# Performance work log

Hardware: AMD Instinct MI355X
Metric: run time of the kernel (lower is better)

The kernel has to match this reference:

```python
import jax, jax.numpy as jnp
import numpy as np

N, C, M, P, FL = 2, 512, 8, 1, 4
SPATIAL = [(100, 100), (50, 50), (25, 25), (13, 13)]
S = sum(h * w for h, w in SPATIAL)
CM = C // M


def grid_sample_zeros(im, grid):
    """torch.nn.functional.grid_sample, bilinear, padding_mode='zeros', align_corners=False.
    im: (B, Cc, H, W); grid: (B, Hg, Wg, 2) with grid[...,0]=x, grid[...,1]=y in [-1,1].
    Returns (B, Cc, Hg, Wg)."""
    B, Cc, H, W = im.shape
    Hg, Wg = grid.shape[1], grid.shape[2]
    x = (grid[..., 0] + 1.0) * (W * 0.5) - 0.5
    y = (grid[..., 1] + 1.0) * (H * 0.5) - 0.5
    x0f = jnp.floor(x)
    y0f = jnp.floor(y)
    wx1 = x - x0f
    wy1 = y - y0f
    wx0 = 1.0 - wx1
    wy0 = 1.0 - wy1
    x0 = x0f.astype(jnp.int32)
    y0 = y0f.astype(jnp.int32)
    flat = im.reshape(B, Cc, H * W)

    def gather(ix, iy):
        valid = ((ix >= 0) & (ix < W) & (iy >= 0) & (iy < H)).astype(im.dtype)
        idx = jnp.clip(iy, 0, H - 1) * W + jnp.clip(ix, 0, W - 1)  # (B,Hg,Wg)
        idx = jnp.broadcast_to(idx.reshape(B, 1, Hg * Wg), (B, Cc, Hg * Wg))
        v = jnp.take_along_axis(flat, idx, axis=2).reshape(B, Cc, Hg, Wg)
        return v * valid[:, None]

    out = (gather(x0, y0) * (wx0 * wy0)[:, None]
           + gather(x0 + 1, y0) * (wx1 * wy0)[:, None]
           + gather(x0, y0 + 1) * (wx0 * wy1)[:, None]
           + gather(x0 + 1, y0 + 1) * (wx1 * wy1)[:, None])
    return out


def setup_inputs() -> dict:
    key = jax.random.key(0)
    ks = jax.random.split(key, 8)
    x = jax.random.normal(ks[0], (N, C, S), jnp.float32)
    pos = jax.random.normal(ks[1], (N, C, S), jnp.float32)
    key_padding_mask = jnp.zeros((N, S), jnp.bool_)
    # valid (W,H) per level; no padding -> full size, scale 1
    valid_sizes = jnp.broadcast_to(
        jnp.array([[w, h] for (h, w) in SPATIAL], jnp.float32)[None], (N, FL, 2))
    valid_scales = jnp.ones((N, FL, 2), jnp.float32)
    s = 1.0 / np.sqrt(C)
    Wv = (jax.random.normal(ks[2], (C, C), jnp.float32) * s)
    bv = jnp.zeros((C,), jnp.float32)
    Wloc = jax.random.normal(ks[3], (M * FL * P * 2, C), jnp.float32) * 0.01
    # torch bias init: head-direction grid, channel layout (M, F, P, 2)
    grid_init = np.array([-1, -1, -1, 0, -1, 1, 0, -1, 0, 1, 1, -1, 1, 0, 1, 1],
                         np.float32).reshape(M, 1, 1, 2)
    grid_init = np.tile(grid_init, (1, FL, P, 1))
    for i in range(P):
        grid_init[:, :, i, :] *= (i + 1)
    bloc = jnp.asarray(grid_init.reshape(-1))
    Ww = jax.random.normal(ks[4], (M * FL * P, C), jnp.float32) * 0.01
    bw = jnp.zeros((M * FL * P,), jnp.float32)
    Wo = (jax.random.normal(ks[5], (C, C), jnp.float32) * s)
    bo = jnp.zeros((C,), jnp.float32)
    scale = jnp.ones((C,), jnp.float32)
    return dict(x=x, pos=pos, key_padding_mask=key_padding_mask,
                valid_sizes=valid_sizes, valid_scales=valid_scales,
                Wv=Wv, bv=bv, Wloc=Wloc, bloc=bloc, Ww=Ww, bw=bw,
                Wo=Wo, bo=bo, scale=scale)


def reference(x, pos, key_padding_mask, valid_sizes, valid_scales,
              Wv, bv, Wloc, bloc, Ww, bw, Wo, bo, scale):
    mask = key_padding_mask[:, None, :]  # (N,1,S)
    x_pos = jnp.where(mask, 0.0, x + pos)
    value = jnp.einsum('oc,ncs->nos', Wv, x) + bv[:, None]
    value = jnp.where(mask, 0.0, value)

    # per-level value maps, split heads: (N*M, C/M, H, W)
    values, cur = [], 0
    for (H, W) in SPATIAL:
        values.append(value[..., cur:cur + H * W].reshape(N * M, CM, H, W))
        cur += H * W

    vs = jnp.repeat(valid_sizes, M, axis=0)          # (NM, F, 2) = repeat_interleave
    vc2 = jnp.repeat(2.0 * valid_scales, M, axis=0)  # (NM, F, 2)

    outs, cur = [], 0
    for lvl, (H, W) in enumerate(SPATIAL):
        L = H * W
        xp = x_pos[..., cur:cur + L]  # (N, C, L)
        cur += L
        # 1x1 convs == per-token linears
        off = jnp.einsum('oc,ncl->nol', Wloc, xp) + bloc[:, None]
        off = off.reshape(N * M, FL, P, 2, L).transpose(0, 1, 2, 4, 3)  # (NM,F,P,L,2)
        w = jnp.einsum('oc,ncl->nol', Ww, xp) + bw[:, None]
        w = jax.nn.softmax(w.reshape(N * M, 1, FL * P, L), axis=2)
        # pixel-center grid of the query level, (L,2) as (x,y)
        ys, xs = jnp.meshgrid(jnp.arange(H, dtype=jnp.float32) + 0.5,
                              jnp.arange(W, dtype=jnp.float32) + 0.5, indexing='ij')
        pre = jnp.stack([xs, ys], -1).reshape(L, 2)
        sc = (vc2 / vs[:, lvl:lvl + 1])[:, :, None, None, :]  # (NM,F,1,1,2)
        grids = off * sc + (pre[None, None, None] * sc - 1.0)  # (NM,F,P,L,2)
        samples = jnp.concatenate(
            [grid_sample_zeros(values[f], grids[:, f]) for f in range(FL)], axis=2)  # (NM,CM,F*P,L)
        out = jnp.sum(samples * w, axis=2).reshape(N, C, L)
        out = jnp.einsum('oc,ncl->nol', Wo, out) + bo[:, None]
        outs.append(out)
    return jnp.concatenate(outs, axis=-1) * scale[None, :, None]
```

## Files before the change

### kernel.cpp

```cpp
#include <hip/hip_runtime.h>
#include <math.h>

#define TOT_S   13294
#define NBATCH  2
#define CCH     512
#define MHEAD   8
#define PITCH   40

typedef short     short8  __attribute__((ext_vector_type(8)));
typedef float     f32x4   __attribute__((ext_vector_type(4)));
typedef unsigned short u16x8 __attribute__((ext_vector_type(8)));
typedef unsigned short u16x4 __attribute__((ext_vector_type(4)));

__device__ __forceinline__ unsigned short f2bf(float f) {
    union { float f; unsigned int u; } v; v.f = f;
    unsigned int r = v.u + 0x7fffu + ((v.u >> 16) & 1u);
    return (unsigned short)(r >> 16);
}
__device__ __forceinline__ float bf2f(unsigned short h) {
    union { unsigned int u; float f; } v; v.u = ((unsigned int)h) << 16;
    return v.f;
}

__global__ void cast_f32_bf16(const float* __restrict__ src,
                              unsigned short* __restrict__ dst, int n4)
{
    const int i = blockIdx.x * blockDim.x + threadIdx.x;
    if (i < n4) {
        const float4 v = *(const float4*)(src + (size_t)i * 4);
        u16x4 o;
        o[0] = f2bf(v.x); o[1] = f2bf(v.y); o[2] = f2bf(v.z); o[3] = f2bf(v.w);
        *(u16x4*)(dst + (size_t)i * 4) = o;
    }
}

__global__ __launch_bounds__(512)
void gemm_val_offw_mfma(const unsigned short* __restrict__ Wb,
                        const unsigned short* __restrict__ Wlb,
                        const unsigned short* __restrict__ Wwb,
                        const float* __restrict__ bv,
                        const float* __restrict__ bloc,
                        const float* __restrict__ bw,
                        const float* __restrict__ x,
                        const float* __restrict__ pos,
                        const unsigned char* __restrict__ mask,
                        unsigned short* __restrict__ valb,
                        float* __restrict__ offw)
{
    __shared__ unsigned short Wl[2][128 * PITCH];
    __shared__ unsigned short Al[2][128 * PITCH];
    const int n  = blockIdx.z;
    const int oby = blockIdx.y;
    const int sb = blockIdx.x * 128;
    const int tid = threadIdx.x;

    const int r    = tid >> 2;
    const int wh   = (tid & 3) >> 1;
    const int segh = (tid & 1) * 16;
    const int sp   = tid & 15;
    const int cgrp = (tid >> 4) & 15;
    const int half = tid >> 8;
    const size_t XLIM = (size_t)NBATCH * CCH * TOT_S - 2;

    const int wave = tid >> 6, lane = tid & 63;
    const int m0 = (wave & 1) * 64, n0 = (wave >> 1) * 32;
    const int row16 = lane & 15, q = lane >> 4;

    if (oby < 4) {
        const int ob = oby * 128;
        const unsigned short* wsrc = Wb + ((size_t)(ob + r)) * CCH + wh * 32 + segh;
        unsigned short* wdst = &Wl[wh][r * PITCH + segh];

        u16x8 w0 = *(const u16x8*)(wsrc);
        u16x8 w1 = *(const u16x8*)(wsrc + 8);
        float2 ax[2][2][2];
#pragma unroll
        for (int kh = 0; kh < 2; ++kh)
#pragma unroll
            for (int cc = 0; cc < 2; ++cc)
#pragma unroll
                for (int jj = 0; jj < 2; ++jj) {
                    size_t off = ((size_t)n * CCH + kh * 32 + 2 * cgrp + cc) * TOT_S
                               + sb + 2 * sp + 32 * (2 * half + jj);
                    off = off > XLIM ? XLIM : off;
                    ax[kh][cc][jj] = *(const float2*)(x + off);
                }

        f32x4 acc[4][2] = {};
        for (int k0 = 0; k0 < CCH; k0 += 64) {
            *(u16x8*)wdst = w0; *(u16x8*)(wdst + 8) = w1;
#pragma unroll
            for (int kh = 0; kh < 2; ++kh)
#pragma unroll
                for (int jj = 0; jj < 2; ++jj)
#pragma unroll
                    for (int i = 0; i < 2; ++i) {
                        const int s = 2 * sp + 32 * (2 * half + jj) + i;
                        const float lo = i ? ax[kh][0][jj].y : ax[kh][0][jj].x;
                        const float hi = i ? ax[kh][1][jj].y : ax[kh][1][jj].x;
                        *(unsigned int*)&Al[kh][(size_t)s * PITCH + 2 * cgrp] =
                            (unsigned int)f2bf(lo) | ((unsigned int)f2bf(hi) << 16);
                    }
            __syncthreads();
            if (k0 + 64 < CCH) {
                w0 = *(const u16x8*)(wsrc + k0 + 64);
                w1 = *(const u16x8*)(wsrc + k0 + 72);
#pragma unroll
                for (int kh = 0; kh < 2; ++kh)
#pragma unroll
                    for (int cc = 0; cc < 2; ++cc)
#pragma unroll
                        for (int jj = 0; jj < 2; ++jj) {
                            size_t off = ((size_t)n * CCH + k0 + 64 + kh * 32
                                          + 2 * cgrp + cc) * TOT_S
                                       + sb + 2 * sp + 32 * (2 * half + jj);
                            off = off > XLIM ? XLIM : off;
                            ax[kh][cc][jj] = *(const float2*)(x + off);
                        }
            }
#pragma unroll
            for (int kh = 0; kh < 2; ++kh) {
                short8 af[4], bfr[2];
#pragma unroll
                for (int mt = 0; mt < 4; ++mt)
                    af[mt] = *(const short8*)&Wl[kh][(m0 + mt * 16 + row16) * PITCH + q * 8];
#pragma unroll
                for (int nt = 0; nt < 2; ++nt)
                    bfr[nt] = *(const short8*)&Al[kh][(n0 + nt * 16 + row16) * PITCH + q * 8];
#pragma unroll
                for (int mt = 0; mt < 4; ++mt)
#pragma unroll
                    for (int nt = 0; nt < 2; ++nt)
                        acc[mt][nt] = __builtin_amdgcn_mfma_f32_16x16x32_bf16(
                            af[mt], bfr[nt], acc[mt][nt], 0, 0, 0);
            }
            __syncthreads();
        }

#pragma unroll
        for (int nt = 0; nt < 2; ++nt) {
            const int s = sb + n0 + nt * 16 + row16;
            if (s >= TOT_S) continue;
            const float msk = mask[(size_t)n * TOT_S + s] ? 0.f : 1.f;
            unsigned short* orow = valb + ((size_t)n * TOT_S + s) * CCH + ob + m0;
#pragma unroll
            for (int mt = 0; mt < 4; ++mt) {
                const f32x4 bvv = *(const f32x4*)(bv + ob + m0 + mt * 16 + q * 4);
                const f32x4 a = acc[mt][nt];
                u16x4 ov;
                ov[0] = f2bf((a[0] + bvv[0]) * msk);
                ov[1] = f2bf((a[1] + bvv[1]) * msk);
                ov[2] = f2bf((a[2] + bvv[2]) * msk);
                ov[3] = f2bf((a[3] + bvv[3]) * msk);
                *(u16x4*)(orow + mt * 16 + q * 4) = ov;
            }
        }
    } else {
        const bool wz = (r >= 96);
        const unsigned short* wsrc =
            (r < 64) ? (Wlb + (size_t)r * CCH + wh * 32 + segh)
                     : (Wwb + (size_t)((r < 96 ? r : 95) - 64) * CCH + wh * 32 + segh);
        unsigned short* wdst = &Wl[wh][r * PITCH + segh];

        float mkm[4];
#pragma unroll
        for (int jj = 0; jj < 2; ++jj)
#pragma unroll
            for (int i = 0; i < 2; ++i) {
                const int s = sb + 2 * sp + 32 * (2 * half + jj) + i;
                const int sc = s < TOT_S ? s : TOT_S - 1;
                mkm[jj * 2 + i] = mask[(size_t)n * TOT_S + sc] ? 0.f : 1.f;
            }

        u16x8 w0 = {}, w1 = {};
        if (!wz) { w0 = *(const u16x8*)(wsrc); w1 = *(const u16x8*)(wsrc + 8); }
        float2 ax[2][2][2], ap[2][2][2];
#pragma unroll
        for (int kh = 0; kh < 2; ++kh)
#pragma unroll
            for (int cc = 0; cc < 2; ++cc)
#pragma unroll
                for (int jj = 0; jj < 2; ++jj) {
                    size_t off = ((size_t)n * CCH + kh * 32 + 2 * cgrp + cc) * TOT_S
                               + sb + 2 * sp + 32 * (2 * half + jj);
                    off = off > XLIM ? XLIM : off;
                    ax[kh][cc][jj] = *(const float2*)(x + off);
                    ap[kh][cc][jj] = *(const float2*)(pos + off);
                }

        f32x4 acc[4][2] = {};
        for (int k0 = 0; k0 < CCH; k0 += 64) {
            *(u16x8*)wdst = w0; *(u16x8*)(wdst + 8) = w1;
#pragma unroll
            for (int kh = 0; kh < 2; ++kh)
#pragma unroll
                for (int jj = 0; jj < 2; ++jj)
#pragma unroll
                    for (int i = 0; i < 2; ++i) {
                        const int s = 2 * sp + 32 * (2 * half + jj) + i;
                        const float lo = (i ? ax[kh][0][jj].y + ap[kh][0][jj].y
                                            : ax[kh][0][jj].x + ap[kh][0][jj].x)
                                         * mkm[jj * 2 + i];
                        const float hi = (i ? ax[kh][1][jj].y + ap[kh][1][jj].y
                                            : ax[kh][1][jj].x + ap[kh][1][jj].x)
                                         * mkm[jj * 2 + i];
                        *(unsigned int*)&Al[kh][(size_t)s * PITCH + 2 * cgrp] =
                            (unsigned int)f2bf(lo) | ((unsigned int)f2bf(hi) << 16);
                    }
            __syncthreads();
            if (k0 + 64 < CCH) {
                if (!wz) {
                    w0 = *(const u16x8*)(wsrc + k0 + 64);
                    w1 = *(const u16x8*)(wsrc + k0 + 72);
                }
#pragma unroll
                for (int kh = 0; kh < 2; ++kh)
#pragma unroll
                    for (int cc = 0; cc < 2; ++cc)
#pragma unroll
                        for (int jj = 0; jj < 2; ++jj) {
                            size_t off = ((size_t)n * CCH + k0 + 64 + kh * 32
                                          + 2 * cgrp + cc) * TOT_S
                                       + sb + 2 * sp + 32 * (2 * half + jj);
                            off = off > XLIM ? XLIM : off;
                            ax[kh][cc][jj] = *(const float2*)(x + off);
                            ap[kh][cc][jj] = *(const float2*)(pos + off);
                        }
            }
#pragma unroll
            for (int kh = 0; kh < 2; ++kh) {
                short8 af[4], bfr[2];
#pragma unroll
                for (int mt = 0; mt < 4; ++mt)
                    af[mt] = *(const short8*)&Wl[kh][(m0 + mt * 16 + row16) * PITCH + q * 8];
#pragma unroll
                for (int nt = 0; nt < 2; ++nt)
                    bfr[nt] = *(const short8*)&Al[kh][(n0 + nt * 16 + row16) * PITCH + q * 8];
#pragma unroll
                for (int mt = 0; mt < 4; ++mt)
#pragma unroll
                    for (int nt = 0; nt < 2; ++nt)
                        acc[mt][nt] = __builtin_amdgcn_mfma_f32_16x16x32_bf16(
                            af[mt], bfr[nt], acc[mt][nt], 0, 0, 0);
            }
            __syncthreads();
        }

#pragma unroll
        for (int nt = 0; nt < 2; ++nt) {
            const int s = sb + n0 + nt * 16 + row16;
            if (s >= TOT_S) continue;
            float* orow = offw + ((size_t)n * TOT_S + s) * 96;
#pragma unroll
            for (int mt = 0; mt < 4; ++mt) {
                const int o = m0 + mt * 16 + q * 4;
                if (o < 96) {
                    const float* bsrc = (o < 64) ? (bloc + o) : (bw + o - 64);
                    const f32x4 bb = *(const f32x4*)bsrc;
                    f32x4 v = acc[mt][nt];
                    v[0] += bb[0]; v[1] += bb[1]; v[2] += bb[2]; v[3] += bb[3];
                    *(f32x4*)(orow + o) = v;
                }
            }
        }
    }
}

__global__ __launch_bounds__(256)
void sample_attn(const unsigned short* __restrict__ value,
                 const float* __restrict__ offw,
                 const float* __restrict__ vsizes,
                 const float* __restrict__ vscales,
                 unsigned short* __restrict__ samp)
{
    const int lane = threadIdx.x;
    const int item = blockIdx.x * blockDim.y + threadIdx.y;
    const int total = NBATCH * TOT_S;
    if (item >= total) return;
    const int s = item % TOT_S;
    const int n = item / TOT_S;
    const int m = lane >> 3;

    int lvl; float prex, prey;
    if (s < 10000)      { lvl = 0; const int l = s;         const int qq = l / 100; prey = qq + 0.5f; prex = (l - qq * 100) + 0.5f; }
    else if (s < 12500) { lvl = 1; const int l = s - 10000; const int qq = l / 50;  prey = qq + 0.5f; prex = (l - qq * 50)  + 0.5f; }
    else if (s < 13125) { lvl = 2; const int l = s - 12500; const int qq = l / 25;  prey = qq + 0.5f; prex = (l - qq * 25)  + 0.5f; }
    else                { lvl = 3; const int l = s - 13125; const int qq = l / 13;  prey = qq + 0.5f; prex = (l - qq * 13)  + 0.5f; }

    const float* ow = offw + ((size_t)n * TOT_S + s) * 96;

    const float w0 = ow[64 + m * 4 + 0], w1 = ow[64 + m * 4 + 1];
    const float w2 = ow[64 + m * 4 + 2], w3 = ow[64 + m * 4 + 3];
    const float mx = fmaxf(fmaxf(w0, w1), fmaxf(w2, w3));
    const float e0 = expf(w0 - mx), e1 = expf(w1 - mx), e2 = expf(w2 - mx), e3 = expf(w3 - mx);
    const float inv = 1.f / (e0 + e1 + e2 + e3);
    const float wgt[4] = { e0 * inv, e1 * inv, e2 * inv, e3 * inv };

    const int HS[4]  = { 100, 50, 25, 13 };
    const int WS[4]  = { 100, 50, 25, 13 };
    const int CUR[4] = { 0, 10000, 12500, 13125 };

    const float invsx = 1.f / vsizes[((n * 4) + lvl) * 2 + 0];
    const float invsy = 1.f / vsizes[((n * 4) + lvl) * 2 + 1];
    const unsigned short* vbase = value + (size_t)n * TOT_S * CCH + lane * 8;

    float acc[8] = {};
#pragma unroll
    for (int f = 0; f < 4; ++f) {
        const float offx = ow[(m * 4 + f) * 2 + 0];
        const float offy = ow[(m * 4 + f) * 2 + 1];
        const float scx = 2.f * vscales[((n * 4) + f) * 2 + 0] * invsx;
        const float scy = 2.f * vscales[((n * 4) + f) * 2 + 1] * invsy;
        const int Wf = WS[f], Hf = HS[f], cf = CUR[f];
        const float xi = (offx + prex) * scx * (Wf * 0.5f) - 0.5f;
        const float yi = (offy + prey) * scy * (Hf * 0.5f) - 0.5f;
        const float x0f = floorf(xi), y0f = floorf(yi);
        const float wx1 = xi - x0f, wy1 = yi - y0f;
        const float wx0 = 1.f - wx1, wy0 = 1.f - wy1;
        const int x0 = (int)x0f, y0 = (int)y0f;
        const bool xin0 = (x0 >= 0) && (x0 < Wf);
        const bool xin1 = (x0 + 1 >= 0) && (x0 + 1 < Wf);
        const bool yin0 = (y0 >= 0) && (y0 < Hf);
        const bool yin1 = (y0 + 1 >= 0) && (y0 + 1 < Hf);
        const float cw00 = (xin0 && yin0) ? wgt[f] * wx0 * wy0 : 0.f;
        const float cw10 = (xin1 && yin0) ? wgt[f] * wx1 * wy0 : 0.f;
        const float cw01 = (xin0 && yin1) ? wgt[f] * wx0 * wy1 : 0.f;
        const float cw11 = (xin1 && yin1) ? wgt[f] * wx1 * wy1 : 0.f;
        const int x0c = min(max(x0, 0), Wf - 1);
        const int x1c = min(max(x0 + 1, 0), Wf - 1);
        const int y0c = min(max(y0, 0), Hf - 1);
        const int y1c = min(max(y0 + 1, 0), Hf - 1);
        const unsigned short* row0 = vbase + (size_t)(cf + y0c * Wf) * CCH;
        const unsigned short* row1 = vbase + (size_t)(cf + y1c * Wf) * CCH;
        const u16x8 v00 = *(const u16x8*)(row0 + (size_t)x0c * CCH);
        const u16x8 v10 = *(const u16x8*)(row0 + (size_t)x1c * CCH);
        const u16x8 v01 = *(const u16x8*)(row1 + (size_t)x0c * CCH);
        const u16x8 v11 = *(const u16x8*)(row1 + (size_t)x1c * CCH);
#pragma unroll
        for (int j = 0; j < 8; ++j) {
            acc[j] += cw00 * bf2f(v00[j]) + cw10 * bf2f(v10[j])
                    + cw01 * bf2f(v01[j]) + cw11 * bf2f(v11[j]);
        }
    }

    u16x8 ov;
#pragma unroll
    for (int j = 0; j < 8; ++j) ov[j] = f2bf(acc[j]);
    *(u16x8*)(samp + ((size_t)n * TOT_S + s) * CCH + lane * 8) = ov;
}

__global__ __launch_bounds__(512)
void gemm_out_mfma(const unsigned short* __restrict__ Wob,
                   const unsigned short* __restrict__ Sampb,
                   const float* __restrict__ bo, const float* __restrict__ scale,
                   float* __restrict__ out)
{
    __shared__ unsigned short Sl[2][128 * PITCH];
    __shared__ unsigned short Wl[2][128 * PITCH];
    const int n  = blockIdx.z;
    const int ob = blockIdx.y * 128;
    const int sb = blockIdx.x * 128;
    const int tid = threadIdx.x;
    const int r    = tid >> 2;
    const int wh   = (tid & 3) >> 1;
    const int segh = (tid & 1) * 16;
    const int sr = min(sb + r, TOT_S - 1);
    const unsigned short* ssrc = Sampb + ((size_t)n * TOT_S + sr) * CCH + wh * 32 + segh;
    const unsigned short* wsrc = Wob + ((size_t)(ob + r)) * CCH + wh * 32 + segh;
    unsigned short* sdst = &Sl[wh][r * PITCH + segh];
    unsigned short* wdst = &Wl[wh][r * PITCH + segh];

    const int wave = tid >> 6, lane = tid & 63;
    const int m0 = (wave & 1) * 64, n0 = (wave >> 1) * 32;
    const int row16 = lane & 15, q = lane >> 4;

    u16x8 s0v = *(const u16x8*)(ssrc);
    u16x8 s1v = *(const u16x8*)(ssrc + 8);
    u16x8 w0v = *(const u16x8*)(wsrc);
    u16x8 w1v = *(const u16x8*)(wsrc + 8);

    f32x4 acc[4][2] = {};
    for (int k0 = 0; k0 < CCH; k0 += 64) {
        *(u16x8*)sdst = s0v; *(u16x8*)(sdst + 8) = s1v;
        *(u16x8*)wdst = w0v; *(u16x8*)(wdst + 8) = w1v;
        __syncthreads();
        if (k0 + 64 < CCH) {
            s0v = *(const u16x8*)(ssrc + k0 + 64);
            s1v = *(const u16x8*)(ssrc + k0 + 72);
            w0v = *(const u16x8*)(wsrc + k0 + 64);
            w1v = *(const u16x8*)(wsrc + k0 + 72);
        }
#pragma unroll
        for (int kh = 0; kh < 2; ++kh) {
            short8 af[4], bfr[2];
#pragma unroll
            for (int mt = 0; mt < 4; ++mt)
                af[mt] = *(const short8*)&Sl[kh][(m0 + mt * 16 + row16) * PITCH + q * 8];
#pragma unroll
            for (int nt = 0; nt < 2; ++nt)
                bfr[nt] = *(const short8*)&Wl[kh][(n0 + nt * 16 + row16) * PITCH + q * 8];
#pragma unroll
            for (int mt = 0; mt < 4; ++mt)
#pragma unroll
                for (int nt = 0; nt < 2; ++nt)
                    acc[mt][nt] = __builtin_amdgcn_mfma_f32_16x16x32_bf16(
                        af[mt], bfr[nt], acc[mt][nt], 0, 0, 0);
        }
        __syncthreads();
    }

#pragma unroll
    for (int nt = 0; nt < 2; ++nt) {
        const int o = ob + n0 + nt * 16 + row16;
        const float bo_ = bo[o];
        const float sc_ = scale[o];
        float* orow = out + ((size_t)n * CCH + o) * (size_t)TOT_S;
#pragma unroll
        for (int mt = 0; mt < 4; ++mt) {
            const int s0 = sb + m0 + mt * 16 + q * 4;
            const f32x4 a = acc[mt][nt];
            if (s0 + 3 < TOT_S) {
                float2 v0 = make_float2((a[0] + bo_) * sc_, (a[1] + bo_) * sc_);
                float2 v1 = make_float2((a[2] + bo_) * sc_, (a[3] + bo_) * sc_);
                *(float2*)(orow + s0) = v0;
                *(float2*)(orow + s0 + 2) = v1;
            } else {
                for (int i = 0; i < 4; ++i)
                    if (s0 + i < TOT_S) orow[s0 + i] = (a[i] + bo_) * sc_;
            }
        }
    }
}

extern "C" void kernel_launch(void* const* d_in, const int* in_sizes, int n_in,
                              void* d_out, int out_size, void* d_ws, size_t ws_size,
                              hipStream_t stream)
{
    const float* x     = (const float*)d_in[0];
    const float* pos   = (const float*)d_in[1];
    const unsigned char* mask = (const unsigned char*)d_in[2];
    const float* vsz   = (const float*)d_in[3];
    const float* vsc   = (const float*)d_in[4];
    const float* Wv    = (const float*)d_in[5];
    const float* bv    = (const float*)d_in[6];
    const float* Wloc  = (const float*)d_in[7];
    const float* bloc  = (const float*)d_in[8];
    const float* Ww    = (const float*)d_in[9];
    const float* bw    = (const float*)d_in[10];
    const float* Wo    = (const float*)d_in[11];
    const float* bo    = (const float*)d_in[12];
    const float* scale = (const float*)d_in[13];
    float* out = (float*)d_out;

    const size_t SC = (size_t)TOT_S * CCH;
    unsigned short* valb  = (unsigned short*)d_ws;
    unsigned short* sampb = valb  + 2 * SC;
    float* offw = (float*)(sampb + 2 * SC);
    unsigned short* wvb = (unsigned short*)(offw + 2 * (size_t)TOT_S * 96);
    unsigned short* wob = wvb + 512 * 512;
    unsigned short* wlb = wob + 512 * 512;
    unsigned short* wwb = wlb + 64 * 512;

    cast_f32_bf16<<<256, 256, 0, stream>>>(Wv,   wvb, 512 * 512 / 4);
    cast_f32_bf16<<<256, 256, 0, stream>>>(Wo,   wob, 512 * 512 / 4);
    cast_f32_bf16<<<32,  256, 0, stream>>>(Wloc, wlb, 64 * 512 / 4);
    cast_f32_bf16<<<16,  256, 0, stream>>>(Ww,   wwb, 32 * 512 / 4);

    const int sTiles = (TOT_S + 127) / 128;

    gemm_val_offw_mfma<<<dim3(sTiles, 5, NBATCH), 512, 0, stream>>>(
        wvb, wlb, wwb, bv, bloc, bw, x, pos, mask, valb, offw);

    const int items = NBATCH * TOT_S;
    sample_attn<<<(items + 3) / 4, dim3(64, 4), 0, stream>>>(valb, offw, vsz, vsc, sampb);

    gemm_out_mfma<<<dim3(sTiles, CCH / 128, NBATCH), 512, 0, stream>>>(
        wob, sampb, bo, scale, out);
}
```

Measured before the change: 285.2 us.

## Use direct global-to-LDS loads with XOR swizzle in output GEMM, merge weight casts

The output projection GEMM now stages its tiles with global_load_lds 16-byte direct copies into double-buffered, XOR-swizzled LDS tiles instead of going through registers into a padded layout. This drops the register round-trip and one barrier per k-step, and lets the next tile's copy overlap the MFMAs. The four weight-cast launches are also merged into one kernel to cut launch overhead. The risk is LDS bank conflicts or wait-count ordering around the async copies.

```diff
diff --git a/kernel.cpp b/kernel.cpp
--- a/kernel.cpp
+++ b/kernel.cpp
@@ -12,6 +12,9 @@
 typedef unsigned short u16x8 __attribute__((ext_vector_type(8)));
 typedef unsigned short u16x4 __attribute__((ext_vector_type(4)));
 
+typedef __attribute__((address_space(1))) const unsigned int glb_u32;
+typedef __attribute__((address_space(3))) unsigned int lds_u32;
+
 __device__ __forceinline__ unsigned short f2bf(float f) {
     union { float f; unsigned int u; } v; v.f = f;
     unsigned int r = v.u + 0x7fffu + ((v.u >> 16) & 1u);
@@ -22,16 +25,24 @@
     return v.f;
 }
 
-__global__ void cast_f32_bf16(const float* __restrict__ src,
-                              unsigned short* __restrict__ dst, int n4)
+__global__ __launch_bounds__(256)
+void cast_all_f32_bf16(const float* __restrict__ Wv, const float* __restrict__ Wo,
+                       const float* __restrict__ Wloc, const float* __restrict__ Ww,
+                       unsigned short* __restrict__ wvb, unsigned short* __restrict__ wob,
+                       unsigned short* __restrict__ wlb, unsigned short* __restrict__ wwb)
 {
     const int i = blockIdx.x * blockDim.x + threadIdx.x;
-    if (i < n4) {
-        const float4 v = *(const float4*)(src + (size_t)i * 4);
-        u16x4 o;
-        o[0] = f2bf(v.x); o[1] = f2bf(v.y); o[2] = f2bf(v.z); o[3] = f2bf(v.w);
-        *(u16x4*)(dst + (size_t)i * 4) = o;
-    }
+    const float* src; unsigned short* dst; int base;
+    if      (i < 65536)  { src = Wv;   dst = wvb; base = 0; }
+    else if (i < 131072) { src = Wo;   dst = wob; base = 65536; }
+    else if (i < 139264) { src = Wloc; dst = wlb; base = 131072; }
+    else if (i < 143360) { src = Ww;   dst = wwb; base = 139264; }
+    else return;
+    const int j = i - base;
+    const float4 v = *(const float4*)(src + (size_t)j * 4);
+    u16x4 o;
+    o[0] = f2bf(v.x); o[1] = f2bf(v.y); o[2] = f2bf(v.z); o[3] = f2bf(v.w);
+    *(u16x4*)(dst + (size_t)j * 4) = o;
 }
 
 __global__ __launch_bounds__(512)
@@ -355,50 +366,56 @@
                    const float* __restrict__ bo, const float* __restrict__ scale,
                    float* __restrict__ out)
 {
-    __shared__ unsigned short Sl[2][128 * PITCH];
-    __shared__ unsigned short Wl[2][128 * PITCH];
+    __shared__ unsigned short Sl[2][2][128 * 32];
+    __shared__ unsigned short Wl[2][2][128 * 32];
     const int n  = blockIdx.z;
     const int ob = blockIdx.y * 128;
     const int sb = blockIdx.x * 128;
     const int tid = threadIdx.x;
-    const int r    = tid >> 2;
-    const int wh   = (tid & 3) >> 1;
-    const int segh = (tid & 1) * 16;
-    const int sr = min(sb + r, TOT_S - 1);
-    const unsigned short* ssrc = Sampb + ((size_t)n * TOT_S + sr) * CCH + wh * 32 + segh;
-    const unsigned short* wsrc = Wob + ((size_t)(ob + r)) * CCH + wh * 32 + segh;
-    unsigned short* sdst = &Sl[wh][r * PITCH + segh];
-    unsigned short* wdst = &Wl[wh][r * PITCH + segh];
-
     const int wave = tid >> 6, lane = tid & 63;
     const int m0 = (wave & 1) * 64, n0 = (wave >> 1) * 32;
     const int row16 = lane & 15, q = lane >> 4;
 
-    u16x8 s0v = *(const u16x8*)(ssrc);
-    u16x8 s1v = *(const u16x8*)(ssrc + 8);
-    u16x8 w0v = *(const u16x8*)(wsrc);
-    u16x8 w1v = *(const u16x8*)(wsrc + 8);
+    const int row_st = wave * 16 + (lane >> 2);
+    const int q_st   = (lane & 3) ^ ((row_st >> 1) & 3);
+    const int s_g    = min(sb + row_st, TOT_S - 1);
+    const unsigned short* sgbase =
+        Sampb + ((size_t)n * TOT_S + s_g) * CCH + q_st * 8;
+    const unsigned short* wgbase =
+        Wob + ((size_t)(ob + row_st)) * CCH + q_st * 8;
+    const int ldsoff = wave * 512;
+
+    const int qx = (q ^ ((row16 >> 1) & 3)) * 8;
+
+#define GL16(gp, lp)                                                          \
+    __builtin_amdgcn_global_load_lds((glb_u32*)(gp), (lds_u32*)(lp), 16, 0, 0)
+
+#pragma unroll
+    for (int kh = 0; kh < 2; ++kh) {
+        GL16(sgbase + kh * 32, &Sl[0][kh][ldsoff]);
+        GL16(wgbase + kh * 32, &Wl[0][kh][ldsoff]);
+    }
+    __syncthreads();
 
     f32x4 acc[4][2] = {};
+    int cur = 0;
     for (int k0 = 0; k0 < CCH; k0 += 64) {
-        *(u16x8*)sdst = s0v; *(u16x8*)(sdst + 8) = s1v;
-        *(u16x8*)wdst = w0v; *(u16x8*)(wdst + 8) = w1v;
-        __syncthreads();
         if (k0 + 64 < CCH) {
-            s0v = *(const u16x8*)(ssrc + k0 + 64);
-            s1v = *(const u16x8*)(ssrc + k0 + 72);
-            w0v = *(const u16x8*)(wsrc + k0 + 64);
-            w1v = *(const u16x8*)(wsrc + k0 + 72);
+#pragma unroll
+            for (int kh = 0; kh < 2; ++kh) {
+                GL16(sgbase + k0 + 64 + kh * 32, &Sl[cur ^ 1][kh][ldsoff]);
+                GL16(wgbase + k0 + 64 + kh * 32, &Wl[cur ^ 1][kh][ldsoff]);
+            }
         }
 #pragma unroll
         for (int kh = 0; kh < 2; ++kh) {
             short8 af[4], bfr[2];
 #pragma unroll
             for (int mt = 0; mt < 4; ++mt)
-                af[mt] = *(const short8*)&Sl[kh][(m0 + mt * 16 + row16) * PITCH + q * 8];
+                af[mt] = *(const short8*)&Sl[cur][kh][(m0 + mt * 16 + row16) * 32 + qx];
 #pragma unroll
             for (int nt = 0; nt < 2; ++nt)
-                bfr[nt] = *(const short8*)&Wl[kh][(n0 + nt * 16 + row16) * PITCH + q * 8];
+                bfr[nt] = *(const short8*)&Wl[cur][kh][(n0 + nt * 16 + row16) * 32 + qx];
 #pragma unroll
             for (int mt = 0; mt < 4; ++mt)
 #pragma unroll
@@ -407,7 +424,9 @@
                         af[mt], bfr[nt], acc[mt][nt], 0, 0, 0);
         }
         __syncthreads();
+        cur ^= 1;
     }
+#undef GL16
 
 #pragma unroll
     for (int nt = 0; nt < 2; ++nt) {
@@ -461,10 +480,8 @@
     unsigned short* wlb = wob + 512 * 512;
     unsigned short* wwb = wlb + 64 * 512;
 
-    cast_f32_bf16<<<256, 256, 0, stream>>>(Wv,   wvb, 512 * 512 / 4);
-    cast_f32_bf16<<<256, 256, 0, stream>>>(Wo,   wob, 512 * 512 / 4);
-    cast_f32_bf16<<<32,  256, 0, stream>>>(Wloc, wlb, 64 * 512 / 4);
-    cast_f32_bf16<<<16,  256, 0, stream>>>(Ww,   wwb, 32 * 512 / 4);
+    cast_all_f32_bf16<<<560, 256, 0, stream>>>(Wv, Wo, Wloc, Ww,
+                                               wvb, wob, wlb, wwb);
 
     const int sTiles = (TOT_S + 127) / 128;
 
```

Result: faster. 277.9 us (-2.5%).
